# Performance work log

Hardware: AMD Instinct MI355X
Metric: run time of the kernel (lower is better)

## Reference

```python
import jax, jax.numpy as jnp
import numpy as np

N_NODES = 100000
HIDDEN = 64
N_LAYERS = 4
N_EDGES = 800000
EPS = 1e-5  # equinox RMSNorm default


def rmsnorm(x, w):
    # per-node RMSNorm over last dim, learned scale, no bias
    inv = jax.lax.rsqrt(jnp.mean(x * x, axis=-1, keepdims=True) + EPS)
    return x * inv * w


def setup_inputs() -> dict:
    key = jax.random.key(0)
    ks = jax.random.split(key, 5)
    x = jax.random.normal(ks[0], (N_NODES, HIDDEN), dtype=jnp.float32)
    # eqx Linear weight (out,in), init ~ U(-1/sqrt(in), 1/sqrt(in)); randn*scale is fine for a baseline
    scale = 1.0 / np.sqrt(HIDDEN)
    conv_w = jax.random.normal(ks[1], (N_LAYERS, HIDDEN, HIDDEN), dtype=jnp.float32) * scale
    hid_w = jax.random.normal(ks[2], (N_LAYERS, HIDDEN, HIDDEN), dtype=jnp.float32) * scale
    conv_norm_w = jnp.ones((N_LAYERS, HIDDEN), dtype=jnp.float32)
    hid_norm_w = jnp.ones((N_LAYERS, HIDDEN), dtype=jnp.float32)
    row = jax.random.randint(ks[3], (N_EDGES,), 0, N_NODES, dtype=jnp.int32)
    col = jax.random.randint(ks[4], (N_EDGES,), 0, N_NODES, dtype=jnp.int32)
    return {"x": x, "conv_w": conv_w, "conv_norm_w": conv_norm_w,
            "hid_w": hid_w, "hid_norm_w": hid_norm_w, "row": row, "col": col}


def reference(x, conv_w, conv_norm_w, hid_w, hid_norm_w, row, col):
    n_nodes = x.shape[0]

    def step(h, params):
        cw, cnw, hw, hnw = params
        # GConvLayer: linear (no bias) -> relu -> sparse adjacency aggregation -> residual RMSNorm
        m = jax.nn.relu(h @ cw.T)                                  # [n_nodes, d]
        agg = jax.ops.segment_sum(m[col], row, num_segments=n_nodes)  # a @ m (unweighted COO)
        h = rmsnorm(h + agg, cnw)
        # HiddenLayer: linear -> relu -> residual RMSNorm
        y = jax.nn.relu(h @ hw.T)
        h = rmsnorm(h + y, hnw)
        return h, None

    x, _ = jax.lax.scan(step, x, (conv_w, conv_norm_w, hid_w, hid_norm_w))
    return x
```

## Files before the change

kernel.cpp:

```cpp
#include <hip/hip_runtime.h>
#include <hip/hip_bf16.h>

#define HIDDEN 64
#define EPS 1e-5f
#define NPB 64
#define WST 72

typedef __attribute__((ext_vector_type(8))) short bf16x8;
typedef __attribute__((ext_vector_type(4))) float f32x4;

__device__ __forceinline__ unsigned short f2b(float x) {
    __hip_bfloat16 b = __float2bfloat16(x);
    return *(unsigned short*)&b;
}
__device__ __forceinline__ float b2f(unsigned short u) {
    unsigned int ui = (unsigned int)u << 16;
    return *(float*)&ui;
}


__global__ __launch_bounds__(256) void hist_rank_kernel(const int* __restrict__ row,
                                                        int* __restrict__ cnt,
                                                        int* __restrict__ erank, int e) {
    int stride = gridDim.x * blockDim.x;
    for (int i = blockIdx.x * blockDim.x + threadIdx.x; i < e; i += stride) {
        int r = row[i];
        erank[i] = atomicAdd(&cnt[r], 1);
    }
}

__global__ __launch_bounds__(256) void block_sum_kernel(const int* __restrict__ cnt,
                                                        int* __restrict__ bsum, int n) {
    __shared__ int wsum[4];
    int tid = threadIdx.x;
    int i = blockIdx.x * 256 + tid;
    int v = (i < n) ? cnt[i] : 0;
#pragma unroll
    for (int off = 32; off > 0; off >>= 1) v += __shfl_xor(v, off, 64);
    if ((tid & 63) == 0) wsum[tid >> 6] = v;
    __syncthreads();
    if (tid == 0) bsum[blockIdx.x] = wsum[0] + wsum[1] + wsum[2] + wsum[3];
}

__global__ __launch_bounds__(1024) void scan_bsum_kernel(int* __restrict__ bsum, int nb,
                                                         int* __restrict__ total_out) {
    __shared__ int wsum[16];
    __shared__ int wexcl[16];
    int tid = threadIdx.x;
    int lane = tid & 63;
    int w = tid >> 6;
    int v = (tid < nb) ? bsum[tid] : 0;
    int sc = v;
#pragma unroll
    for (int off = 1; off < 64; off <<= 1) {
        int t = __shfl_up(sc, off, 64);
        if (lane >= off) sc += t;
    }
    if (lane == 63) wsum[w] = sc;
    __syncthreads();
    if (tid == 0) {
        int a = 0;
#pragma unroll
        for (int j = 0; j < 16; j++) { wexcl[j] = a; a += wsum[j]; }
        *total_out = a;
    }
    __syncthreads();
    if (tid < nb) bsum[tid] = wexcl[w] + (sc - v);
}

__global__ __launch_bounds__(256) void scan_final_kernel(const int* __restrict__ cnt,
                                                         const int* __restrict__ bexcl,
                                                         int* __restrict__ row_ptr, int n) {
    __shared__ int wsum[4];
    __shared__ int wexcl[4];
    int tid = threadIdx.x;
    int lane = tid & 63;
    int w = tid >> 6;
    int i = blockIdx.x * 256 + tid;
    int v = (i < n) ? cnt[i] : 0;
    int sc = v;
#pragma unroll
    for (int off = 1; off < 64; off <<= 1) {
        int t = __shfl_up(sc, off, 64);
        if (lane >= off) sc += t;
    }
    if (lane == 63) wsum[w] = sc;
    __syncthreads();
    if (tid == 0) {
        int a = 0;
#pragma unroll
        for (int j = 0; j < 4; j++) { wexcl[j] = a; a += wsum[j]; }
    }
    __syncthreads();
    if (i < n) row_ptr[i] = bexcl[blockIdx.x] + wexcl[w] + (sc - v);
}

__global__ __launch_bounds__(256) void fill_kernel(const int* __restrict__ row,
                                                   const int* __restrict__ col,
                                                   const int* __restrict__ row_ptr,
                                                   const int* __restrict__ erank,
                                                   int* __restrict__ ecol, int e, int n) {
    int cls = blockIdx.x & 7;
    int sub = blockIdx.x >> 3;
    int nsub = gridDim.x >> 3;
    int lo = (int)(((long long)n * cls) >> 3);
    int hi = (int)(((long long)n * (cls + 1)) >> 3);
    for (int i = sub * 256 + threadIdx.x; i < e; i += nsub * 256) {
        int r = row[i];
        if (r >= lo && r < hi) {
            int pos = row_ptr[r] + erank[i];
            ecol[pos] = col[i];
        }
    }
}

__global__ __launch_bounds__(256) void wconv_kernel(const float* __restrict__ cw,
                                                    const float* __restrict__ hw,
                                                    unsigned short* __restrict__ wbt, int L) {
    int idx = blockIdx.x * blockDim.x + threadIdx.x;
    int total = 2 * L * 4096;
    if (idx >= total) return;
    int mat = idx >> 12;
    int rem = idx & 4095;
    const float* src = (mat < L) ? (cw + (size_t)mat * 4096) : (hw + (size_t)(mat - L) * 4096);
    wbt[idx] = f2b(src[rem]);
}


__device__ __forceinline__ void mfma_tile(const unsigned short* s_a,
                                          const unsigned short* s_b,
                                          int l16, int quad, int wbase, f32x4 acc[4]) {
    const unsigned short* ap = &s_a[(size_t)(wbase + l16) * WST + quad * 8];
    const unsigned short* bp = &s_b[(size_t)l16 * WST + quad * 8];
#pragma unroll
    for (int kt = 0; kt < 2; kt++) {
        bf16x8 a = *(const bf16x8*)(ap + kt * 32);
#pragma unroll
        for (int nt = 0; nt < 4; nt++) {
            bf16x8 b = *(const bf16x8*)(bp + (size_t)nt * 16 * WST + kt * 32);
            acc[nt] = __builtin_amdgcn_mfma_f32_16x16x32_bf16(a, b, acc[nt], 0, 0, 0);
        }
    }
}

__device__ __forceinline__ void stage_wb(const unsigned short* __restrict__ wsrc,
                                         unsigned short* s_wb, int tid) {
    for (int i = tid; i < 512; i += 256) {
        int r = i >> 3, seg = i & 7;
        *(uint4*)(&s_wb[r * WST + seg * 8]) = ((const uint4*)(wsrc + r * 64))[seg];
    }
}


__global__ __launch_bounds__(256) void mm_relu_kernel(const float* __restrict__ h,
                                                      const unsigned short* __restrict__ wb,
                                                      __hip_bfloat16* __restrict__ m, int n) {
    __shared__ unsigned short s_hb[NPB * WST];
    __shared__ unsigned short s_wb[64 * WST];
    int tid = threadIdx.x;
    int base = blockIdx.x * NPB;
    stage_wb(wb, s_wb, tid);
    for (int i = tid; i < 512; i += 256) {
        int r = i >> 3, seg = i & 7;
        uint2 p = make_uint2(0u, 0u);
        if (base + r < n) {
            const float4* hp = (const float4*)(h + (size_t)(base + r) * HIDDEN + seg * 8);
            float4 ha = hp[0], hb = hp[1];
            p.x = (unsigned int)f2b(ha.x) | ((unsigned int)f2b(ha.y) << 16);
            p.y = (unsigned int)f2b(ha.z) | ((unsigned int)f2b(ha.w) << 16);
            unsigned int pz = (unsigned int)f2b(hb.x) | ((unsigned int)f2b(hb.y) << 16);
            unsigned int pw = (unsigned int)f2b(hb.z) | ((unsigned int)f2b(hb.w) << 16);
            *(uint4*)(&s_hb[r * WST + seg * 8]) = make_uint4(p.x, p.y, pz, pw);
        } else {
            *(uint4*)(&s_hb[r * WST + seg * 8]) = make_uint4(0u, 0u, 0u, 0u);
        }
    }
    __syncthreads();
    int lane = tid & 63, wave = tid >> 6;
    int quad = lane >> 4, l16 = lane & 15;
    int wbase = wave * 16;
    f32x4 acc[4];
    acc[0] = (f32x4){0.f,0.f,0.f,0.f}; acc[1] = (f32x4){0.f,0.f,0.f,0.f};
    acc[2] = (f32x4){0.f,0.f,0.f,0.f}; acc[3] = (f32x4){0.f,0.f,0.f,0.f};
    mfma_tile(s_hb, s_wb, l16, quad, wbase, acc);
    unsigned short* mo = (unsigned short*)m;
#pragma unroll
    for (int r = 0; r < 4; r++) {
        int node = base + wbase + quad * 4 + r;
        if (node < n) {
#pragma unroll
            for (int nt = 0; nt < 4; nt++)
                mo[(size_t)node * HIDDEN + nt * 16 + l16] = f2b(fmaxf(acc[nt][r], 0.f));
        }
    }
}

__global__ __launch_bounds__(256) void aggregate_kernel(const float* __restrict__ h,
                                                        const __hip_bfloat16* __restrict__ m,
                                                        const int* __restrict__ row_ptr,
                                                        const int* __restrict__ ecol,
                                                        const float* __restrict__ nw,
                                                        float* __restrict__ out,
                                                        __hip_bfloat16* __restrict__ hb, int n) {
    int lane = threadIdx.x & 63;
    int wave = (blockIdx.x * blockDim.x + threadIdx.x) >> 6;
    int half = lane >> 5;
    int sl = lane & 31;
    int node = 2 * wave + half;
    if (node >= n) return;
    int beg = row_ptr[node];
    int end = row_ptr[node + 1];
    float2 s = *(const float2*)(h + (size_t)node * HIDDEN + 2 * sl);
    const unsigned short* mi = (const unsigned short*)m;
    float ax[8], ay[8];
#pragma unroll
    for (int q = 0; q < 8; q++) { ax[q] = 0.f; ay[q] = 0.f; }
    int sbase = half * 32;
    for (int b0 = beg; b0 < end; b0 += 32) {
        int idx = b0 + sl;
        int myc = ecol[idx < end ? idx : end - 1];
        int cnt = end - b0;
        if (cnt > 32) cnt = 32;
        for (int q0 = 0; q0 < cnt; q0 += 8) {
            int c[8];
#pragma unroll
            for (int j = 0; j < 8; j++) c[j] = __shfl(myc, sbase + q0 + j, 64);
            unsigned int u[8];
#pragma unroll
            for (int j = 0; j < 8; j++)
                u[j] = *(const unsigned int*)(mi + (size_t)c[j] * HIDDEN + 2 * sl);
#pragma unroll
            for (int j = 0; j < 8; j++) {
                bool ok = (q0 + j) < cnt;
                ax[j] += ok ? b2f((unsigned short)(u[j] & 0xffffu)) : 0.f;
                ay[j] += ok ? b2f((unsigned short)(u[j] >> 16)) : 0.f;
            }
        }
    }
    s.x += (((ax[0] + ax[1]) + (ax[2] + ax[3])) + ((ax[4] + ax[5]) + (ax[6] + ax[7])));
    s.y += (((ay[0] + ay[1]) + (ay[2] + ay[3])) + ((ay[4] + ay[5]) + (ay[6] + ay[7])));
    float ss = s.x * s.x + s.y * s.y;
#pragma unroll
    for (int off = 16; off > 0; off >>= 1) ss += __shfl_xor(ss, off, 64);
    float inv = rsqrtf(ss * (1.0f / 64.0f) + EPS);
    float2 w2 = *(const float2*)(nw + 2 * sl);
    float2 o2 = make_float2(s.x * inv * w2.x, s.y * inv * w2.y);
    *(float2*)(out + (size_t)node * HIDDEN + 2 * sl) = o2;
    unsigned int pb = (unsigned int)f2b(o2.x) | ((unsigned int)f2b(o2.y) << 16);
    *(unsigned int*)((unsigned short*)hb + (size_t)node * HIDDEN + 2 * sl) = pb;
}


__global__ __launch_bounds__(256) void hidden_next_kernel(float* __restrict__ h,
                                                          const __hip_bfloat16* __restrict__ hb,
                                                          const unsigned short* __restrict__ hwb,
                                                          const unsigned short* cwb_next,
                                                          const float* __restrict__ hnw,
                                                          __hip_bfloat16* m_out, int n) {
    __shared__ unsigned short s_hb[NPB * WST];
    __shared__ unsigned short s_wb[64 * WST];
    __shared__ unsigned short s_wb2[64 * WST];
    int tid = threadIdx.x;
    int base = blockIdx.x * NPB;
    stage_wb(hwb, s_wb, tid);
    if (cwb_next) stage_wb(cwb_next, s_wb2, tid);
    const unsigned short* hbs = (const unsigned short*)hb;
    for (int i = tid; i < 512; i += 256) {
        int r = i >> 3, seg = i & 7;
        uint4 p = make_uint4(0u, 0u, 0u, 0u);
        if (base + r < n) p = ((const uint4*)(hbs + (size_t)(base + r) * HIDDEN))[seg];
        *(uint4*)(&s_hb[r * WST + seg * 8]) = p;
    }
    __syncthreads();

    int lane = tid & 63, wave = tid >> 6;
    int quad = lane >> 4, l16 = lane & 15;
    int wbase = wave * 16;

    f32x4 acc[4];
    acc[0] = (f32x4){0.f,0.f,0.f,0.f}; acc[1] = (f32x4){0.f,0.f,0.f,0.f};
    acc[2] = (f32x4){0.f,0.f,0.f,0.f}; acc[3] = (f32x4){0.f,0.f,0.f,0.f};
    mfma_tile(s_hb, s_wb, l16, quad, wbase, acc);

    float hv[4][4];
    float ssq[4] = {0.f, 0.f, 0.f, 0.f};
#pragma unroll
    for (int r = 0; r < 4; r++) {
        int node = base + wbase + quad * 4 + r;
        bool ok = node < n;
#pragma unroll
        for (int nt = 0; nt < 4; nt++) {
            float hres = ok ? h[(size_t)node * HIDDEN + nt * 16 + l16] : 0.f;
            float v = hres + fmaxf(acc[nt][r], 0.f);
            hv[r][nt] = v;
            ssq[r] += v * v;
        }
    }
#pragma unroll
    for (int mk = 1; mk <= 8; mk <<= 1) {
#pragma unroll
        for (int r = 0; r < 4; r++) ssq[r] += __shfl_xor(ssq[r], mk, 64);
    }
    float nwv[4];
#pragma unroll
    for (int nt = 0; nt < 4; nt++) nwv[nt] = hnw[nt * 16 + l16];
#pragma unroll
    for (int r = 0; r < 4; r++) {
        float inv = rsqrtf(ssq[r] * (1.0f / 64.0f) + EPS);
#pragma unroll
        for (int nt = 0; nt < 4; nt++) hv[r][nt] *= inv * nwv[nt];
    }
#pragma unroll
    for (int r = 0; r < 4; r++) {
        int node = base + wbase + quad * 4 + r;
        if (node < n) {
#pragma unroll
            for (int nt = 0; nt < 4; nt++)
                h[(size_t)node * HIDDEN + nt * 16 + l16] = hv[r][nt];
        }
    }

    if (!m_out) return;

#pragma unroll
    for (int r = 0; r < 4; r++) {
        int nl = wbase + quad * 4 + r;
#pragma unroll
        for (int nt = 0; nt < 4; nt++)
            s_hb[nl * WST + nt * 16 + l16] = f2b(hv[r][nt]);
    }

    f32x4 acc2[4];
    acc2[0] = (f32x4){0.f,0.f,0.f,0.f}; acc2[1] = (f32x4){0.f,0.f,0.f,0.f};
    acc2[2] = (f32x4){0.f,0.f,0.f,0.f}; acc2[3] = (f32x4){0.f,0.f,0.f,0.f};
    mfma_tile(s_hb, s_wb2, l16, quad, wbase, acc2);
    unsigned short* mo = (unsigned short*)m_out;
#pragma unroll
    for (int r = 0; r < 4; r++) {
        int node = base + wbase + quad * 4 + r;
        if (node < n) {
#pragma unroll
            for (int nt = 0; nt < 4; nt++)
                mo[(size_t)node * HIDDEN + nt * 16 + l16] = f2b(fmaxf(acc2[nt][r], 0.f));
        }
    }
}


static inline size_t align_up(size_t x, size_t a) { return (x + a - 1) & ~(a - 1); }

extern "C" void kernel_launch(void* const* d_in, const int* in_sizes, int n_in,
                              void* d_out, int out_size, void* d_ws, size_t ws_size,
                              hipStream_t stream) {
    const float* x       = (const float*)d_in[0];
    const float* conv_w  = (const float*)d_in[1];
    const float* conv_nw = (const float*)d_in[2];
    const float* hid_w   = (const float*)d_in[3];
    const float* hid_nw  = (const float*)d_in[4];
    const int*   row     = (const int*)d_in[5];
    const int*   col     = (const int*)d_in[6];
    float* out = (float*)d_out;

    const int n = in_sizes[0] / HIDDEN;
    const int e = in_sizes[5];
    const int L = in_sizes[1] / 4096;

    size_t off = 0;
    char* ws = (char*)d_ws;
    __hip_bfloat16* mA = (__hip_bfloat16*)(ws + off); off = align_up(off + (size_t)n * HIDDEN * 2, 16);
    __hip_bfloat16* mB = (__hip_bfloat16*)(ws + off); off = align_up(off + (size_t)n * HIDDEN * 2, 16);
    __hip_bfloat16* hbb = (__hip_bfloat16*)(ws + off); off = align_up(off + (size_t)n * HIDDEN * 2, 16);
    unsigned short* wbt = (unsigned short*)(ws + off); off = align_up(off + (size_t)2 * L * 4096 * 2, 16);
    int* row_ptr = (int*)(ws + off);           off = align_up(off + (size_t)(n + 1) * 4, 16);
    int* cnt = (int*)(ws + off);               off = align_up(off + (size_t)n * 4, 16);
    int* bsum = (int*)(ws + off);              off = align_up(off + (size_t)1024 * 4, 16);
    int* erank = (int*)(ws + off);             off = align_up(off + (size_t)e * 4, 16);
    int* ecol = (int*)(ws + off);              off = align_up(off + (size_t)e * 4, 16);

    const int nb = (n + 255) / 256;

    hipMemsetAsync(cnt, 0, (size_t)n * 4, stream);
    hist_rank_kernel<<<1024, 256, 0, stream>>>(row, cnt, erank, e);
    block_sum_kernel<<<nb, 256, 0, stream>>>(cnt, bsum, n);
    scan_bsum_kernel<<<1, 1024, 0, stream>>>(bsum, nb, row_ptr + n);
    scan_final_kernel<<<nb, 256, 0, stream>>>(cnt, bsum, row_ptr, n);
    fill_kernel<<<1024, 256, 0, stream>>>(row, col, row_ptr, erank, ecol, e, n);

    wconv_kernel<<<(2 * L * 4096 + 255) / 256, 256, 0, stream>>>(conv_w, hid_w, wbt, L);

    const int blocks = (n + NPB - 1) / NPB;
    const int agg_blocks = ((n + 1) / 2 * 64 + 255) / 256;

    mm_relu_kernel<<<blocks, 256, 0, stream>>>(x, wbt, mA, n);

    const __hip_bfloat16* mi = mA;
    __hip_bfloat16* mo = mB;
    const float* hcur = x;
    for (int l = 0; l < L; l++) {
        aggregate_kernel<<<agg_blocks, 256, 0, stream>>>(hcur, mi, row_ptr, ecol,
                                                         conv_nw + (size_t)l * HIDDEN, out, hbb, n);
        hidden_next_kernel<<<blocks, 256, 0, stream>>>(
            out, hbb, wbt + (size_t)(L + l) * 4096,
            (l < L - 1) ? (wbt + (size_t)(l + 1) * 4096) : nullptr,
            hid_nw + (size_t)l * HIDDEN,
            (l < L - 1) ? mo : nullptr, n);
        __hip_bfloat16* tmp = (__hip_bfloat16*)mi; mi = mo; mo = tmp;
        hcur = out;
    }
}
```

Before: 316.2 us.

## Carry hidden state in bf16 between layers and widen aggregate lanes

```diff
diff --git a/kernel.cpp b/kernel.cpp
--- a/kernel.cpp
+++ b/kernel.cpp
@@ -162,15 +162,15 @@
     stage_wb(wb, s_wb, tid);
     for (int i = tid; i < 512; i += 256) {
         int r = i >> 3, seg = i & 7;
-        uint2 p = make_uint2(0u, 0u);
         if (base + r < n) {
             const float4* hp = (const float4*)(h + (size_t)(base + r) * HIDDEN + seg * 8);
             float4 ha = hp[0], hb = hp[1];
+            uint4 p;
             p.x = (unsigned int)f2b(ha.x) | ((unsigned int)f2b(ha.y) << 16);
             p.y = (unsigned int)f2b(ha.z) | ((unsigned int)f2b(ha.w) << 16);
-            unsigned int pz = (unsigned int)f2b(hb.x) | ((unsigned int)f2b(hb.y) << 16);
-            unsigned int pw = (unsigned int)f2b(hb.z) | ((unsigned int)f2b(hb.w) << 16);
-            *(uint4*)(&s_hb[r * WST + seg * 8]) = make_uint4(p.x, p.y, pz, pw);
+            p.z = (unsigned int)f2b(hb.x) | ((unsigned int)f2b(hb.y) << 16);
+            p.w = (unsigned int)f2b(hb.z) | ((unsigned int)f2b(hb.w) << 16);
+            *(uint4*)(&s_hb[r * WST + seg * 8]) = p;
         } else {
             *(uint4*)(&s_hb[r * WST + seg * 8]) = make_uint4(0u, 0u, 0u, 0u);
         }
@@ -195,67 +195,81 @@
     }
 }
 
-__global__ __launch_bounds__(256) void aggregate_kernel(const float* __restrict__ h,
+__global__ __launch_bounds__(256) void aggregate_kernel(const float* hf,
+                                                        const __hip_bfloat16* hb_in,
                                                         const __hip_bfloat16* __restrict__ m,
                                                         const int* __restrict__ row_ptr,
                                                         const int* __restrict__ ecol,
                                                         const float* __restrict__ nw,
-                                                        float* __restrict__ out,
-                                                        __hip_bfloat16* __restrict__ hb, int n) {
+                                                        __hip_bfloat16* __restrict__ hb_out,
+                                                        int n) {
     int lane = threadIdx.x & 63;
     int wave = (blockIdx.x * blockDim.x + threadIdx.x) >> 6;
-    int half = lane >> 5;
-    int sl = lane & 31;
-    int node = 2 * wave + half;
+    int grp = lane >> 4;
+    int sl = lane & 15;
+    int node = 4 * wave + grp;
     if (node >= n) return;
     int beg = row_ptr[node];
     int end = row_ptr[node + 1];
-    float2 s = *(const float2*)(h + (size_t)node * HIDDEN + 2 * sl);
+    float s0, s1, s2, s3;
+    if (hf) {
+        float4 v = *(const float4*)(hf + (size_t)node * HIDDEN + 4 * sl);
+        s0 = v.x; s1 = v.y; s2 = v.z; s3 = v.w;
+    } else {
+        uint2 u = *(const uint2*)((const unsigned short*)hb_in + (size_t)node * HIDDEN + 4 * sl);
+        s0 = b2f((unsigned short)(u.x & 0xffffu)); s1 = b2f((unsigned short)(u.x >> 16));
+        s2 = b2f((unsigned short)(u.y & 0xffffu)); s3 = b2f((unsigned short)(u.y >> 16));
+    }
     const unsigned short* mi = (const unsigned short*)m;
-    float ax[8], ay[8];
-#pragma unroll
-    for (int q = 0; q < 8; q++) { ax[q] = 0.f; ay[q] = 0.f; }
-    int sbase = half * 32;
-    for (int b0 = beg; b0 < end; b0 += 32) {
+    float a0[8], a1[8], a2[8], a3[8];
+#pragma unroll
+    for (int q = 0; q < 8; q++) { a0[q] = 0.f; a1[q] = 0.f; a2[q] = 0.f; a3[q] = 0.f; }
+    int sbase = grp * 16;
+    for (int b0 = beg; b0 < end; b0 += 16) {
         int idx = b0 + sl;
         int myc = ecol[idx < end ? idx : end - 1];
         int cnt = end - b0;
-        if (cnt > 32) cnt = 32;
+        if (cnt > 16) cnt = 16;
         for (int q0 = 0; q0 < cnt; q0 += 8) {
             int c[8];
 #pragma unroll
             for (int j = 0; j < 8; j++) c[j] = __shfl(myc, sbase + q0 + j, 64);
-            unsigned int u[8];
+            uint2 u[8];
 #pragma unroll
             for (int j = 0; j < 8; j++)
-                u[j] = *(const unsigned int*)(mi + (size_t)c[j] * HIDDEN + 2 * sl);
+                u[j] = *(const uint2*)(mi + (size_t)c[j] * HIDDEN + 4 * sl);
 #pragma unroll
             for (int j = 0; j < 8; j++) {
                 bool ok = (q0 + j) < cnt;
-                ax[j] += ok ? b2f((unsigned short)(u[j] & 0xffffu)) : 0.f;
-                ay[j] += ok ? b2f((unsigned short)(u[j] >> 16)) : 0.f;
+                a0[j] += ok ? b2f((unsigned short)(u[j].x & 0xffffu)) : 0.f;
+                a1[j] += ok ? b2f((unsigned short)(u[j].x >> 16)) : 0.f;
+                a2[j] += ok ? b2f((unsigned short)(u[j].y & 0xffffu)) : 0.f;
+                a3[j] += ok ? b2f((unsigned short)(u[j].y >> 16)) : 0.f;
             }
         }
     }
-    s.x += (((ax[0] + ax[1]) + (ax[2] + ax[3])) + ((ax[4] + ax[5]) + (ax[6] + ax[7])));
-    s.y += (((ay[0] + ay[1]) + (ay[2] + ay[3])) + ((ay[4] + ay[5]) + (ay[6] + ay[7])));
-    float ss = s.x * s.x + s.y * s.y;
-#pragma unroll
-    for (int off = 16; off > 0; off >>= 1) ss += __shfl_xor(ss, off, 64);
+    s0 += (((a0[0] + a0[1]) + (a0[2] + a0[3])) + ((a0[4] + a0[5]) + (a0[6] + a0[7])));
+    s1 += (((a1[0] + a1[1]) + (a1[2] + a1[3])) + ((a1[4] + a1[5]) + (a1[6] + a1[7])));
+    s2 += (((a2[0] + a2[1]) + (a2[2] + a2[3])) + ((a2[4] + a2[5]) + (a2[6] + a2[7])));
+    s3 += (((a3[0] + a3[1]) + (a3[2] + a3[3])) + ((a3[4] + a3[5]) + (a3[6] + a3[7])));
+    float ss = s0 * s0 + s1 * s1 + s2 * s2 + s3 * s3;
+#pragma unroll
+    for (int off = 8; off > 0; off >>= 1) ss += __shfl_xor(ss, off, 64);
     float inv = rsqrtf(ss * (1.0f / 64.0f) + EPS);
-    float2 w2 = *(const float2*)(nw + 2 * sl);
-    float2 o2 = make_float2(s.x * inv * w2.x, s.y * inv * w2.y);
-    *(float2*)(out + (size_t)node * HIDDEN + 2 * sl) = o2;
-    unsigned int pb = (unsigned int)f2b(o2.x) | ((unsigned int)f2b(o2.y) << 16);
-    *(unsigned int*)((unsigned short*)hb + (size_t)node * HIDDEN + 2 * sl) = pb;
-}
-
-
-__global__ __launch_bounds__(256) void hidden_next_kernel(float* __restrict__ h,
-                                                          const __hip_bfloat16* __restrict__ hb,
+    float4 w4 = *(const float4*)(nw + 4 * sl);
+    uint2 pb;
+    pb.x = (unsigned int)f2b(s0 * inv * w4.x) | ((unsigned int)f2b(s1 * inv * w4.y) << 16);
+    pb.y = (unsigned int)f2b(s2 * inv * w4.z) | ((unsigned int)f2b(s3 * inv * w4.w) << 16);
+    *(uint2*)((unsigned short*)hb_out + (size_t)node * HIDDEN + 4 * sl) = pb;
+}
+
+
+__global__ __launch_bounds__(256) void hidden_next_kernel(const __hip_bfloat16* __restrict__ hb_in,
                                                           const unsigned short* __restrict__ hwb,
                                                           const unsigned short* cwb_next,
                                                           const float* __restrict__ hnw,
+                                                          float* out_f32,
+                                                          __hip_bfloat16* hb_new,
                                                           __hip_bfloat16* m_out, int n) {
     __shared__ unsigned short s_hb[NPB * WST];
     __shared__ unsigned short s_wb[64 * WST];
@@ -264,7 +278,7 @@
     int base = blockIdx.x * NPB;
     stage_wb(hwb, s_wb, tid);
     if (cwb_next) stage_wb(cwb_next, s_wb2, tid);
-    const unsigned short* hbs = (const unsigned short*)hb;
+    const unsigned short* hbs = (const unsigned short*)hb_in;
     for (int i = tid; i < 512; i += 256) {
         int r = i >> 3, seg = i & 7;
         uint4 p = make_uint4(0u, 0u, 0u, 0u);
@@ -286,11 +300,10 @@
     float ssq[4] = {0.f, 0.f, 0.f, 0.f};
 #pragma unroll
     for (int r = 0; r < 4; r++) {
-        int node = base + wbase + quad * 4 + r;
-        bool ok = node < n;
+        int nl = wbase + quad * 4 + r;
 #pragma unroll
         for (int nt = 0; nt < 4; nt++) {
-            float hres = ok ? h[(size_t)node * HIDDEN + nt * 16 + l16] : 0.f;
+            float hres = b2f(s_hb[(size_t)nl * WST + nt * 16 + l16]);
             float v = hres + fmaxf(acc[nt][r], 0.f);
             hv[r][nt] = v;
             ssq[r] += v * v;
@@ -310,13 +323,27 @@
 #pragma unroll
         for (int nt = 0; nt < 4; nt++) hv[r][nt] *= inv * nwv[nt];
     }
-#pragma unroll
-    for (int r = 0; r < 4; r++) {
-        int node = base + wbase + quad * 4 + r;
-        if (node < n) {
-#pragma unroll
-            for (int nt = 0; nt < 4; nt++)
-                h[(size_t)node * HIDDEN + nt * 16 + l16] = hv[r][nt];
+    if (out_f32) {
+#pragma unroll
+        for (int r = 0; r < 4; r++) {
+            int node = base + wbase + quad * 4 + r;
+            if (node < n) {
+#pragma unroll
+                for (int nt = 0; nt < 4; nt++)
+                    out_f32[(size_t)node * HIDDEN + nt * 16 + l16] = hv[r][nt];
+            }
+        }
+    }
+    if (hb_new) {
+        unsigned short* ho = (unsigned short*)hb_new;
+#pragma unroll
+        for (int r = 0; r < 4; r++) {
+            int node = base + wbase + quad * 4 + r;
+            if (node < n) {
+#pragma unroll
+                for (int nt = 0; nt < 4; nt++)
+                    ho[(size_t)node * HIDDEN + nt * 16 + l16] = f2b(hv[r][nt]);
+            }
         }
     }
 
@@ -327,7 +354,7 @@
         int nl = wbase + quad * 4 + r;
 #pragma unroll
         for (int nt = 0; nt < 4; nt++)
-            s_hb[nl * WST + nt * 16 + l16] = f2b(hv[r][nt]);
+            s_hb[(size_t)nl * WST + nt * 16 + l16] = f2b(hv[r][nt]);
     }
 
     f32x4 acc2[4];
@@ -367,9 +394,10 @@
 
     size_t off = 0;
     char* ws = (char*)d_ws;
-    __hip_bfloat16* mA = (__hip_bfloat16*)(ws + off); off = align_up(off + (size_t)n * HIDDEN * 2, 16);
-    __hip_bfloat16* mB = (__hip_bfloat16*)(ws + off); off = align_up(off + (size_t)n * HIDDEN * 2, 16);
-    __hip_bfloat16* hbb = (__hip_bfloat16*)(ws + off); off = align_up(off + (size_t)n * HIDDEN * 2, 16);
+    __hip_bfloat16* mA = (__hip_bfloat16*)(ws + off);  off = align_up(off + (size_t)n * HIDDEN * 2, 16);
+    __hip_bfloat16* mB = (__hip_bfloat16*)(ws + off);  off = align_up(off + (size_t)n * HIDDEN * 2, 16);
+    __hip_bfloat16* hb1 = (__hip_bfloat16*)(ws + off); off = align_up(off + (size_t)n * HIDDEN * 2, 16);
+    __hip_bfloat16* hb2 = (__hip_bfloat16*)(ws + off); off = align_up(off + (size_t)n * HIDDEN * 2, 16);
     unsigned short* wbt = (unsigned short*)(ws + off); off = align_up(off + (size_t)2 * L * 4096 * 2, 16);
     int* row_ptr = (int*)(ws + off);           off = align_up(off + (size_t)(n + 1) * 4, 16);
     int* cnt = (int*)(ws + off);               off = align_up(off + (size_t)n * 4, 16);
@@ -389,22 +417,24 @@
     wconv_kernel<<<(2 * L * 4096 + 255) / 256, 256, 0, stream>>>(conv_w, hid_w, wbt, L);
 
     const int blocks = (n + NPB - 1) / NPB;
-    const int agg_blocks = ((n + 1) / 2 * 64 + 255) / 256;
+    const int agg_blocks = ((n + 3) / 4 * 64 + 255) / 256;
 
     mm_relu_kernel<<<blocks, 256, 0, stream>>>(x, wbt, mA, n);
 
     const __hip_bfloat16* mi = mA;
     __hip_bfloat16* mo = mB;
-    const float* hcur = x;
     for (int l = 0; l < L; l++) {
-        aggregate_kernel<<<agg_blocks, 256, 0, stream>>>(hcur, mi, row_ptr, ecol,
-                                                         conv_nw + (size_t)l * HIDDEN, out, hbb, n);
+        aggregate_kernel<<<agg_blocks, 256, 0, stream>>>(
+            (l == 0) ? x : nullptr, (l == 0) ? nullptr : hb2, mi, row_ptr, ecol,
+            conv_nw + (size_t)l * HIDDEN, hb1, n);
+        bool last = (l == L - 1);
         hidden_next_kernel<<<blocks, 256, 0, stream>>>(
-            out, hbb, wbt + (size_t)(L + l) * 4096,
-            (l < L - 1) ? (wbt + (size_t)(l + 1) * 4096) : nullptr,
+            hb1, wbt + (size_t)(L + l) * 4096,
+            last ? nullptr : (wbt + (size_t)(l + 1) * 4096),
             hid_nw + (size_t)l * HIDDEN,
-            (l < L - 1) ? mo : nullptr, n);
+            last ? out : nullptr,
+            last ? nullptr : hb2,
+            last ? nullptr : mo, n);
         __hip_bfloat16* tmp = (__hip_bfloat16*)mi; mi = mo; mo = tmp;
-        hcur = out;
-    }
-}
+    }
+}
```

Measured after the change: 291.1 us. 7.9% less time.
